# Optimization experiments

Measured on AMD Instinct MI355X. Metric: run time of the kernel, lower is better.

Reference implementation:

```python
import jax, jax.numpy as jnp
import numpy as np

B, T, C = 2, 2048, 1024
H, HS, RD = 16, 64, 64
KV_R, Q_R = 256, 384


def _rope_tables(T, dim):
    # standard RoPE angle tables, shape [T, dim]
    half = dim // 2
    inv_freq = 1.0 / (10000.0 ** (np.arange(0, half, dtype=np.float32) / half))
    t = np.arange(T, dtype=np.float32)
    ang = np.outer(t, inv_freq)  # [T, half]
    ang = np.concatenate([ang, ang], axis=-1)  # [T, dim]
    return jnp.asarray(np.cos(ang)), jnp.asarray(np.sin(ang))


def setup_inputs() -> dict:
    key = jax.random.key(0)
    ks = jax.random.split(key, 8)
    cos, sin = _rope_tables(T, RD)
    s = lambda fan_in: 1.0 / np.sqrt(fan_in)
    return {
        "x": jax.random.normal(ks[0], (B, T, C), jnp.float32),
        "cos": cos,
        "sin": sin,
        "W_kv_down": jax.random.normal(ks[1], (C, KV_R), jnp.float32) * s(C),
        "W_kv_up": jax.random.normal(ks[2], (KV_R, H * HS), jnp.float32) * s(KV_R),
        "W_k_rope": jax.random.normal(ks[3], (KV_R, H * RD), jnp.float32) * s(KV_R),
        "W_q_down": jax.random.normal(ks[4], (C, Q_R), jnp.float32) * s(C),
        "W_q_up": jax.random.normal(ks[5], (Q_R, H * HS), jnp.float32) * s(Q_R),
        "W_q_rope": jax.random.normal(ks[6], (Q_R, H * RD), jnp.float32) * s(Q_R),
        "W_out": jax.random.normal(ks[7], (H * HS, C), jnp.float32) * s(H * HS),
    }


def _apply_rope(x, cos, sin):
    # x: [B,H,T,D]; cos/sin: [T,D] broadcast
    d = x.shape[-1]
    x1, x2 = x[..., : d // 2], x[..., d // 2 :]
    rotated = jnp.concatenate([-x2, x1], axis=-1)
    return x * cos + rotated * sin


def reference(x, cos, sin, W_kv_down, W_kv_up, W_k_rope, W_q_down, W_q_up, W_q_rope, W_out):
    Bx, Tx, Cx = x.shape
    to_heads = lambda z, d: jnp.swapaxes(z.reshape(Bx, Tx, H, d), 1, 2)  # [B,H,T,d]

    latent_kv = x @ W_kv_down                      # [B,T,KV_R]
    kv_up = latent_kv @ W_kv_up                    # [B,T,H*HS]
    v = to_heads(kv_up, HS)
    k_content = to_heads(kv_up, HS)                # same projection used for k and v
    k_rope = _apply_rope(to_heads(latent_kv @ W_k_rope, RD), cos[:Tx], sin[:Tx])

    latent_q = x @ W_q_down                        # [B,T,Q_R]
    q_content = to_heads(latent_q @ W_q_up, HS)
    q_rope = _apply_rope(to_heads(latent_q @ W_q_rope, RD), cos[:Tx], sin[:Tx])

    q = jnp.concatenate([q_content, q_rope], axis=-1)  # [B,H,T,HS+RD]
    k = jnp.concatenate([k_content, k_rope], axis=-1)

    att = jnp.einsum("bhqd,bhkd->bhqk", q, k) * (HS ** -0.5)
    causal = jnp.tril(jnp.ones((Tx, Tx), bool))
    att = jnp.where(causal, att, -jnp.inf)
    att = jax.nn.softmax(att, axis=-1)             # dropout is eval-mode identity
    y = jnp.einsum("bhqk,bhkd->bhqd", att, v)      # [B,H,T,HS]
    y = jnp.swapaxes(y, 1, 2).reshape(Bx, Tx, H * HS)
    return y @ W_out
```

## Files before the change

### kernel.cpp

```cpp
#include <hip/hip_runtime.h>
#include <stdint.h>

typedef unsigned short u16;
typedef __bf16 bf16x8 __attribute__((ext_vector_type(8)));
typedef float f32x4 __attribute__((ext_vector_type(4)));

#define B_ 2
#define T_ 2048

__device__ __forceinline__ u16 f2b(float f) {
  unsigned u = __float_as_uint(f);
  u += 0x7fffu + ((u >> 16) & 1u);
  return (u16)(u >> 16);
}
__device__ __forceinline__ float b2f(u16 v) {
  return __uint_as_float(((unsigned)v) << 16);
}
__device__ __forceinline__ unsigned cvt_pk(float lo, float hi) {
  unsigned r;
  asm("v_cvt_pk_bf16_f32 %0, %1, %2" : "=v"(r) : "v"(lo), "v"(hi));
  return r;
}

using gu32 = __attribute__((address_space(1))) const unsigned int;
using lu32 = __attribute__((address_space(3))) unsigned int;
__device__ __forceinline__ void gl_lds16(const u16* g, u16* l) {
  __builtin_amdgcn_global_load_lds((gu32*)g, (lu32*)l, 16, 0, 0);
}

__global__ __launch_bounds__(256) void conv_x_kernel(const float* __restrict__ in,
                                                     u16* __restrict__ out) {
  int i = (blockIdx.x * 256 + threadIdx.x) * 4;
  float4 v = *reinterpret_cast<const float4*>(in + i);
  union { u16 h[4]; unsigned long long ll; } pk;
  pk.h[0] = f2b(v.x); pk.h[1] = f2b(v.y); pk.h[2] = f2b(v.z); pk.h[3] = f2b(v.w);
  *reinterpret_cast<unsigned long long*>(out + i) = pk.ll;
}

__global__ __launch_bounds__(256) void transpose_w_kernel(const float* __restrict__ W,
                                                          int K, int N,
                                                          u16* __restrict__ Wt,
                                                          int ldt, int row_off) {
  __shared__ float tile[32][33];
  int n0 = blockIdx.x * 32, k0 = blockIdx.y * 32;
  int cx = threadIdx.x, ry = threadIdx.y;
  #pragma unroll
  for (int i = 0; i < 4; i++)
    tile[ry + i * 8][cx] = W[(size_t)(k0 + ry + i * 8) * N + n0 + cx];
  __syncthreads();
  #pragma unroll
  for (int i = 0; i < 4; i++)
    Wt[(size_t)(row_off + n0 + ry + i * 8) * ldt + k0 + cx] = f2b(tile[cx][ry + i * 8]);
}

__global__ __launch_bounds__(256) void gemm_bt(const u16* __restrict__ A, int lda,
                                               const u16* __restrict__ Bt, int ldb,
                                               void* __restrict__ Cout, int ldc,
                                               int K, int f32out, u16* __restrict__ vt) {
  __shared__ u16 As[2][128 * 32];
  __shared__ u16 Bs[2][128 * 32];
  const int tid = threadIdx.x;
  const int wave = tid >> 6, lane = tid & 63;
  const int wr = wave >> 1, wc = wave & 1;
  const int l15 = lane & 15, l4 = lane >> 4;
  const int m0 = blockIdx.y * 128, n0 = blockIdx.x * 128;
  const int lr = lane >> 2;
  const int lc = (lane & 3) * 8;

  f32x4 acc[4][4];
  const f32x4 fzero = {0.f, 0.f, 0.f, 0.f};
  #pragma unroll
  for (int m = 0; m < 4; m++)
    #pragma unroll
    for (int n = 0; n < 4; n++)
      acc[m][n] = fzero;

  const u16* gA  = A  + (size_t)(m0 + wave * 32 + lr) * lda + lc;
  const u16* gA2 = gA + (size_t)16 * lda;
  const u16* gB  = Bt + (size_t)(n0 + wave * 32 + lr) * ldb + lc;
  const u16* gB2 = gB + (size_t)16 * ldb;

  auto stage = [&](int buf, int k0) {
    u16* lA  = &As[buf][(wave * 32) * 32];
    u16* lA2 = &As[buf][(wave * 32 + 16) * 32];
    u16* lB  = &Bs[buf][(wave * 32) * 32];
    u16* lB2 = &Bs[buf][(wave * 32 + 16) * 32];
    gl_lds16(gA + k0, lA);
    gl_lds16(gA2 + k0, lA2);
    gl_lds16(gB + k0, lB);
    gl_lds16(gB2 + k0, lB2);
  };

  stage(0, 0);
  __syncthreads();
  int buf = 0;
  for (int k0 = 0; k0 < K; k0 += 32) {
    if (k0 + 32 < K) stage(buf ^ 1, k0 + 32);
    bf16x8 af[4], bfr[4];
    #pragma unroll
    for (int m = 0; m < 4; m++)
      af[m] = *reinterpret_cast<const bf16x8*>(&As[buf][(wr * 64 + m * 16 + l15) * 32 + l4 * 8]);
    #pragma unroll
    for (int n = 0; n < 4; n++)
      bfr[n] = *reinterpret_cast<const bf16x8*>(&Bs[buf][(wc * 64 + n * 16 + l15) * 32 + l4 * 8]);
    #pragma unroll
    for (int m = 0; m < 4; m++)
      #pragma unroll
      for (int n = 0; n < 4; n++)
        acc[m][n] = __builtin_amdgcn_mfma_f32_16x16x32_bf16(af[m], bfr[n], acc[m][n], 0, 0, 0);
    __syncthreads();
    buf ^= 1;
  }

  const int row_base = m0 + wr * 64 + l4 * 4;
  const int col_base = n0 + wc * 64 + l15;
  if (f32out) {
    float* Cf = (float*)Cout;
    #pragma unroll
    for (int m = 0; m < 4; m++)
      #pragma unroll
      for (int n = 0; n < 4; n++)
        #pragma unroll
        for (int r = 0; r < 4; r++)
          Cf[(size_t)(row_base + m * 16 + r) * ldc + col_base + n * 16] = acc[m][n][r];
  } else {
    u16* Cb = (u16*)Cout;
    #pragma unroll
    for (int m = 0; m < 4; m++)
      #pragma unroll
      for (int n = 0; n < 4; n++)
        #pragma unroll
        for (int r = 0; r < 4; r++)
          Cb[(size_t)(row_base + m * 16 + r) * ldc + col_base + n * 16] = f2b(acc[m][n][r]);
    if (vt) {
      #pragma unroll
      for (int m = 0; m < 4; m++)
        #pragma unroll
        for (int n = 0; n < 4; n++) {
          int col = col_base + n * 16;
          if (col < 1024) {
            int mm = row_base + m * 16;
            int bb = mm >> 11, tt = mm & 2047;
            uint2 pk2;
            pk2.x = cvt_pk(acc[m][n][0], acc[m][n][1]);
            pk2.y = cvt_pk(acc[m][n][2], acc[m][n][3]);
            *reinterpret_cast<uint2*>(&vt[(size_t)(bb * 1024 + col) * 2048 + tt]) = pk2;
          }
        }
    }
  }
}

__global__ __launch_bounds__(256) void rope_kernel(u16* __restrict__ buf,
                                                   const float* __restrict__ cosT,
                                                   const float* __restrict__ sinT) {
  int idx = blockIdx.x * 256 + threadIdx.x;
  int i8 = (idx & 3) * 8;
  int hh = (idx >> 2) & 15;
  int r  = idx >> 6;
  int t  = r & (T_ - 1);
  size_t base = (size_t)r * 2048 + 1024 + hh * 64;
  uint4 pa = *reinterpret_cast<const uint4*>(&buf[base + i8]);
  uint4 pb = *reinterpret_cast<const uint4*>(&buf[base + i8 + 32]);
  const u16* ap = reinterpret_cast<const u16*>(&pa);
  const u16* bp = reinterpret_cast<const u16*>(&pb);
  const float* cp = cosT + t * 64 + i8;
  const float* sp = sinT + t * 64 + i8;
  float y1[8], y2[8];
  #pragma unroll
  for (int j = 0; j < 8; j++) {
    float x1 = b2f(ap[j]), x2 = b2f(bp[j]);
    y1[j] = x1 * cp[j] - x2 * sp[j];
    y2[j] = x2 * cp[j + 32] + x1 * sp[j + 32];
  }
  uint4 o1, o2;
  o1.x = cvt_pk(y1[0], y1[1]); o1.y = cvt_pk(y1[2], y1[3]);
  o1.z = cvt_pk(y1[4], y1[5]); o1.w = cvt_pk(y1[6], y1[7]);
  o2.x = cvt_pk(y2[0], y2[1]); o2.y = cvt_pk(y2[2], y2[3]);
  o2.z = cvt_pk(y2[4], y2[5]); o2.w = cvt_pk(y2[6], y2[7]);
  *reinterpret_cast<uint4*>(&buf[base + i8]) = o1;
  *reinterpret_cast<uint4*>(&buf[base + i8 + 32]) = o2;
}

__global__ __launch_bounds__(256) void attn_kernel(const u16* __restrict__ qo,
                                                   const u16* __restrict__ kvo,
                                                   const u16* __restrict__ vtg,
                                                   u16* __restrict__ yb) {
  __shared__ u16 K_lds[2][64 * 128];
  __shared__ u16 V_lds[2][64 * 64];
  __shared__ u16 P_lds[4][16][72];
  const int tid = threadIdx.x;
  const int wave = tid >> 6, lane = tid & 63;
  const int l15 = lane & 15, l4 = lane >> 4;
  const int bid = blockIdx.x;
  const int bh = bid & 31;
  const int qi = 31 - (bid >> 5);
  const int b = bh >> 4, h = bh & 15;
  const int q0 = qi * 64;
  const int qrow = q0 + wave * 16 + l15;

  const u16* qb = qo + (size_t)(b * T_ + qrow) * 2048 + h * 64;
  bf16x8 qf[4];
  qf[0] = *reinterpret_cast<const bf16x8*>(qb + l4 * 8);
  qf[1] = *reinterpret_cast<const bf16x8*>(qb + 32 + l4 * 8);
  qf[2] = *reinterpret_cast<const bf16x8*>(qb + 1024 + l4 * 8);
  qf[3] = *reinterpret_cast<const bf16x8*>(qb + 1056 + l4 * 8);

  const u16* Kbase = kvo + (size_t)(b * T_) * 2048 + h * 64;
  const u16* Vbase = vtg + (size_t)(b * 1024 + h * 64) * 2048;

  const int krow_i = lane >> 4;
  const int kc2 = (lane & 15) * 16;
  const int vrow_i = lane >> 3;
  const int vc2 = (lane & 7) * 16;

  auto stage = [&](int buf, int kv0) {
    #pragma unroll
    for (int j = 0; j < 4; j++) {
      int row = wave * 16 + j * 4 + krow_i;
      int c2x = kc2 ^ ((row & 7) << 4);
      int cu = c2x >> 1;
      const u16* src = Kbase + (size_t)(kv0 + row) * 2048 + (cu < 64 ? cu : 960 + cu);
      gl_lds16(src, &K_lds[buf][(wave * 16 + j * 4) * 128]);
    }
    #pragma unroll
    for (int j = 0; j < 2; j++) {
      int row = wave * 16 + j * 8 + vrow_i;
      int c2x = vc2 ^ ((row & 7) << 4);
      const u16* src = Vbase + (size_t)row * 2048 + kv0 + (c2x >> 1);
      gl_lds16(src, &V_lds[buf][(wave * 16 + j * 8) * 64]);
    }
  };

  const f32x4 fzero = {0.f, 0.f, 0.f, 0.f};
  f32x4 oT[4];
  #pragma unroll
  for (int f = 0; f < 4; f++) oT[f] = fzero;
  float m_run = -1e30f, l_run = 0.f;

  const int nt = qi + 1;
  stage(0, 0);
  __syncthreads();
  int buf = 0;

  for (int t = 0; t < nt; t++) {
    const int kv0 = t * 64;
    if (t + 1 < nt) stage(buf ^ 1, kv0 + 64);

    const char* Kb = (const char*)&K_lds[buf][0];
    const char* Vb = (const char*)&V_lds[buf][0];

    f32x4 sT[4];
    #pragma unroll
    for (int c = 0; c < 4; c++) sT[c] = fzero;
    #pragma unroll
    for (int c = 0; c < 4; c++) {
      const int krow = c * 16 + l15;
      const int kxm = (krow & 7) << 4;
      #pragma unroll
      for (int s = 0; s < 4; s++) {
        bf16x8 kf = *reinterpret_cast<const bf16x8*>(
            Kb + krow * 256 + ((s * 64 + l4 * 16) ^ kxm));
        sT[c] = __builtin_amdgcn_mfma_f32_16x16x32_bf16(kf, qf[s], sT[c], 0, 0, 0);
      }
    }

    const bool diag = (kv0 == q0);
    float p[4][4];
    float mx = -1e30f;
    #pragma unroll
    for (int c = 0; c < 4; c++)
      #pragma unroll
      for (int r = 0; r < 4; r++) {
        float s = sT[c][r] * 0.125f;
        if (diag) {
          int kv = kv0 + c * 16 + l4 * 4 + r;
          if (kv > qrow) s = -1e30f;
        }
        p[c][r] = s;
        mx = fmaxf(mx, s);
      }
    mx = fmaxf(mx, __shfl_xor(mx, 16));
    mx = fmaxf(mx, __shfl_xor(mx, 32));
    float m_new = fmaxf(m_run, mx);
    float corr = __expf(m_run - m_new);
    float rsum = 0.f;
    #pragma unroll
    for (int c = 0; c < 4; c++)
      #pragma unroll
      for (int r = 0; r < 4; r++) {
        float pe = __expf(p[c][r] - m_new);
        p[c][r] = pe;
        rsum += pe;
      }
    rsum += __shfl_xor(rsum, 16);
    rsum += __shfl_xor(rsum, 32);
    l_run = l_run * corr + rsum;
    m_run = m_new;
    #pragma unroll
    for (int f = 0; f < 4; f++) oT[f] *= corr;

    #pragma unroll
    for (int c = 0; c < 4; c++) {
      uint2 pk2;
      pk2.x = cvt_pk(p[c][0], p[c][1]);
      pk2.y = cvt_pk(p[c][2], p[c][3]);
      *reinterpret_cast<uint2*>(&P_lds[wave][l15][c * 16 + l4 * 4]) = pk2;
    }
    bf16x8 pb0 = *reinterpret_cast<const bf16x8*>(&P_lds[wave][l15][l4 * 8]);
    bf16x8 pb1 = *reinterpret_cast<const bf16x8*>(&P_lds[wave][l15][32 + l4 * 8]);

    #pragma unroll
    for (int f = 0; f < 4; f++) {
      const int vrow = f * 16 + l15;
      const int vxm = (vrow & 7) << 4;
      bf16x8 v0 = *reinterpret_cast<const bf16x8*>(Vb + vrow * 128 + ((l4 * 16) ^ vxm));
      bf16x8 v1 = *reinterpret_cast<const bf16x8*>(Vb + vrow * 128 + ((64 + l4 * 16) ^ vxm));
      oT[f] = __builtin_amdgcn_mfma_f32_16x16x32_bf16(v0, pb0, oT[f], 0, 0, 0);
      oT[f] = __builtin_amdgcn_mfma_f32_16x16x32_bf16(v1, pb1, oT[f], 0, 0, 0);
    }

    __syncthreads();
    buf ^= 1;
  }

  const float inv = 1.f / l_run;
  #pragma unroll
  for (int f = 0; f < 4; f++) {
    uint2 pk2;
    pk2.x = cvt_pk(oT[f][0] * inv, oT[f][1] * inv);
    pk2.y = cvt_pk(oT[f][2] * inv, oT[f][3] * inv);
    *reinterpret_cast<uint2*>(
        &yb[(size_t)(b * T_ + qrow) * 1024 + h * 64 + f * 16 + l4 * 4]) = pk2;
  }
}

extern "C" void kernel_launch(void* const* d_in, const int* in_sizes, int n_in,
                              void* d_out, int out_size, void* d_ws, size_t ws_size,
                              hipStream_t stream) {
  const float* x         = (const float*)d_in[0];
  const float* cosT      = (const float*)d_in[1];
  const float* sinT      = (const float*)d_in[2];
  const float* W_kv_down = (const float*)d_in[3];
  const float* W_kv_up   = (const float*)d_in[4];
  const float* W_k_rope  = (const float*)d_in[5];
  const float* W_q_down  = (const float*)d_in[6];
  const float* W_q_up    = (const float*)d_in[7];
  const float* W_q_rope  = (const float*)d_in[8];
  const float* W_out     = (const float*)d_in[9];
  float* out = (float*)d_out;
  char* ws = (char*)d_ws;

  u16* xb    = (u16*)(ws + 0);
  u16* lat   = (u16*)(ws + 8388608);
  u16* WdT   = (u16*)(ws + 13631488);
  u16* WkvT  = (u16*)(ws + 14942208);
  u16* WqT   = (u16*)(ws + 15990784);
  u16* WoutT = (u16*)(ws + 17563648);
  u16* kvo   = (u16*)(ws + 19660800);
  u16* qo    = (u16*)(ws + 36438016);
  u16* VT    = (u16*)(ws + 53215232);
  u16* yb    = (u16*)(ws + 0);

  dim3 tb(32, 8);
  conv_x_kernel<<<4096, 256, 0, stream>>>(x, xb);
  transpose_w_kernel<<<dim3(8, 32),  tb, 0, stream>>>(W_kv_down, 1024, 256,  WdT,  1024, 0);
  transpose_w_kernel<<<dim3(12, 32), tb, 0, stream>>>(W_q_down,  1024, 384,  WdT,  1024, 256);
  transpose_w_kernel<<<dim3(32, 8),  tb, 0, stream>>>(W_kv_up,   256,  1024, WkvT, 256,  0);
  transpose_w_kernel<<<dim3(32, 8),  tb, 0, stream>>>(W_k_rope,  256,  1024, WkvT, 256,  1024);
  transpose_w_kernel<<<dim3(32, 12), tb, 0, stream>>>(W_q_up,    384,  1024, WqT,  384,  0);
  transpose_w_kernel<<<dim3(32, 12), tb, 0, stream>>>(W_q_rope,  384,  1024, WqT,  384,  1024);
  transpose_w_kernel<<<dim3(32, 32), tb, 0, stream>>>(W_out,     1024, 1024, WoutT, 1024, 0);

  gemm_bt<<<dim3(5, 32), 256, 0, stream>>>(xb, 1024, WdT, 1024, lat, 640, 1024, 0, nullptr);
  gemm_bt<<<dim3(16, 32), 256, 0, stream>>>(lat, 640, WkvT, 256, kvo, 2048, 256, 0, VT);
  gemm_bt<<<dim3(16, 32), 256, 0, stream>>>(lat + 256, 640, WqT, 384, qo, 2048, 384, 0, nullptr);

  rope_kernel<<<1024, 256, 0, stream>>>(kvo, cosT, sinT);
  rope_kernel<<<1024, 256, 0, stream>>>(qo, cosT, sinT);

  attn_kernel<<<1024, 256, 0, stream>>>(qo, kvo, VT, yb);

  gemm_bt<<<dim3(8, 32), 256, 0, stream>>>(yb, 1024, WoutT, 1024, out, 1024, 1024, 1, nullptr);
}
```

Before: 248.9 us.

## Fuse RoPE into GEMM epilogue, batch transposes, enlarge attention tiles, lazy rescale

The seven weight transposes are merged into one launch driven by a job table. RoPE moves into the epilogue of the up-projection GEMMs, which removes the separate read-modify-write rope pass. Attention now uses 512-thread blocks covering 128 query rows and shares each K/V tile across eight waves, skipping tiles above the diagonal per wave. Softmax switches to exp2 with a pre-scaled logit and only rescales when the running max rises past a threshold. The gain comes from fewer launches and less global traffic, at the cost of wave imbalance near the diagonal and a looser softmax rescale that could affect precision.

```diff
diff --git a/kernel.cpp b/kernel.cpp
--- a/kernel.cpp
+++ b/kernel.cpp
@@ -19,6 +19,11 @@
 __device__ __forceinline__ unsigned cvt_pk(float lo, float hi) {
   unsigned r;
   asm("v_cvt_pk_bf16_f32 %0, %1, %2" : "=v"(r) : "v"(lo), "v"(hi));
+  return r;
+}
+__device__ __forceinline__ float ex2(float x) {
+  float r;
+  asm("v_exp_f32 %0, %1" : "=v"(r) : "v"(x));
   return r;
 }
 
@@ -37,26 +42,37 @@
   *reinterpret_cast<unsigned long long*>(out + i) = pk.ll;
 }
 
-__global__ __launch_bounds__(256) void transpose_w_kernel(const float* __restrict__ W,
-                                                          int K, int N,
-                                                          u16* __restrict__ Wt,
-                                                          int ldt, int row_off) {
+struct TJob { const float* src; u16* dst; int K, N, ldt, row_off, blk0; };
+struct TJobs { TJob j[7]; };
+
+__global__ __launch_bounds__(256) void transpose_all_kernel(TJobs jobs) {
   __shared__ float tile[32][33];
-  int n0 = blockIdx.x * 32, k0 = blockIdx.y * 32;
+  int bid = blockIdx.x;
+  int ji = 0;
+  #pragma unroll
+  for (int i = 6; i > 0; --i)
+    if (bid >= jobs.j[i].blk0) { ji = i; break; }
+  const TJob jb = jobs.j[ji];
+  int local = bid - jb.blk0;
+  int nb = jb.N >> 5;
+  int n0 = (local % nb) * 32, k0 = (local / nb) * 32;
   int cx = threadIdx.x, ry = threadIdx.y;
   #pragma unroll
   for (int i = 0; i < 4; i++)
-    tile[ry + i * 8][cx] = W[(size_t)(k0 + ry + i * 8) * N + n0 + cx];
+    tile[ry + i * 8][cx] = jb.src[(size_t)(k0 + ry + i * 8) * jb.N + n0 + cx];
   __syncthreads();
   #pragma unroll
   for (int i = 0; i < 4; i++)
-    Wt[(size_t)(row_off + n0 + ry + i * 8) * ldt + k0 + cx] = f2b(tile[cx][ry + i * 8]);
+    jb.dst[(size_t)(jb.row_off + n0 + ry + i * 8) * jb.ldt + k0 + cx] =
+        f2b(tile[cx][ry + i * 8]);
 }
 
 __global__ __launch_bounds__(256) void gemm_bt(const u16* __restrict__ A, int lda,
                                                const u16* __restrict__ Bt, int ldb,
                                                void* __restrict__ Cout, int ldc,
-                                               int K, int f32out, u16* __restrict__ vt) {
+                                               int K, int mode, u16* __restrict__ vt,
+                                               const float* __restrict__ cosT,
+                                               const float* __restrict__ sinT) {
   __shared__ u16 As[2][128 * 32];
   __shared__ u16 Bs[2][128 * 32];
   const int tid = threadIdx.x;
@@ -81,14 +97,10 @@
   const u16* gB2 = gB + (size_t)16 * ldb;
 
   auto stage = [&](int buf, int k0) {
-    u16* lA  = &As[buf][(wave * 32) * 32];
-    u16* lA2 = &As[buf][(wave * 32 + 16) * 32];
-    u16* lB  = &Bs[buf][(wave * 32) * 32];
-    u16* lB2 = &Bs[buf][(wave * 32 + 16) * 32];
-    gl_lds16(gA + k0, lA);
-    gl_lds16(gA2 + k0, lA2);
-    gl_lds16(gB + k0, lB);
-    gl_lds16(gB2 + k0, lB2);
+    gl_lds16(gA + k0, &As[buf][(wave * 32) * 32]);
+    gl_lds16(gA2 + k0, &As[buf][(wave * 32 + 16) * 32]);
+    gl_lds16(gB + k0, &Bs[buf][(wave * 32) * 32]);
+    gl_lds16(gB2 + k0, &Bs[buf][(wave * 32 + 16) * 32]);
   };
 
   stage(0, 0);
@@ -114,7 +126,8 @@
 
   const int row_base = m0 + wr * 64 + l4 * 4;
   const int col_base = n0 + wc * 64 + l15;
-  if (f32out) {
+
+  if (mode == 1) {
     float* Cf = (float*)Cout;
     #pragma unroll
     for (int m = 0; m < 4; m++)
@@ -123,80 +136,70 @@
         #pragma unroll
         for (int r = 0; r < 4; r++)
           Cf[(size_t)(row_base + m * 16 + r) * ldc + col_base + n * 16] = acc[m][n][r];
-  } else {
-    u16* Cb = (u16*)Cout;
-    #pragma unroll
-    for (int m = 0; m < 4; m++)
-      #pragma unroll
-      for (int n = 0; n < 4; n++)
-        #pragma unroll
-        for (int r = 0; r < 4; r++)
-          Cb[(size_t)(row_base + m * 16 + r) * ldc + col_base + n * 16] = f2b(acc[m][n][r]);
-    if (vt) {
-      #pragma unroll
-      for (int m = 0; m < 4; m++)
-        #pragma unroll
-        for (int n = 0; n < 4; n++) {
-          int col = col_base + n * 16;
-          if (col < 1024) {
-            int mm = row_base + m * 16;
-            int bb = mm >> 11, tt = mm & 2047;
-            uint2 pk2;
-            pk2.x = cvt_pk(acc[m][n][0], acc[m][n][1]);
-            pk2.y = cvt_pk(acc[m][n][2], acc[m][n][3]);
-            *reinterpret_cast<uint2*>(&vt[(size_t)(bb * 1024 + col) * 2048 + tt]) = pk2;
-          }
+    return;
+  }
+
+  if (mode >= 2 && (n0 + wc * 64) >= 1024) {
+    #pragma unroll
+    for (int m = 0; m < 4; m++)
+      #pragma unroll
+      for (int r = 0; r < 4; r++) {
+        int t = (row_base + m * 16 + r) & (T_ - 1);
+        const float* cp = cosT + t * 64 + l15;
+        const float* sp = sinT + t * 64 + l15;
+        float c0 = cp[0], c16 = cp[16], c32 = cp[32], c48 = cp[48];
+        float s0 = sp[0], s16 = sp[16], s32 = sp[32], s48 = sp[48];
+        float x0 = acc[m][0][r], x1 = acc[m][1][r];
+        float x2 = acc[m][2][r], x3 = acc[m][3][r];
+        acc[m][0][r] = x0 * c0 - x2 * s0;
+        acc[m][1][r] = x1 * c16 - x3 * s16;
+        acc[m][2][r] = x2 * c32 + x0 * s32;
+        acc[m][3][r] = x3 * c48 + x1 * s48;
+      }
+  }
+
+  u16* Cb = (u16*)Cout;
+  #pragma unroll
+  for (int m = 0; m < 4; m++)
+    #pragma unroll
+    for (int n = 0; n < 4; n++)
+      #pragma unroll
+      for (int r = 0; r < 4; r++)
+        Cb[(size_t)(row_base + m * 16 + r) * ldc + col_base + n * 16] = f2b(acc[m][n][r]);
+
+  if (mode == 2) {
+    #pragma unroll
+    for (int m = 0; m < 4; m++)
+      #pragma unroll
+      for (int n = 0; n < 4; n++) {
+        int col = col_base + n * 16;
+        if (col < 1024) {
+          int mm = row_base + m * 16;
+          int bb = mm >> 11, tt = mm & 2047;
+          uint2 pk2;
+          pk2.x = cvt_pk(acc[m][n][0], acc[m][n][1]);
+          pk2.y = cvt_pk(acc[m][n][2], acc[m][n][3]);
+          *reinterpret_cast<uint2*>(&vt[(size_t)(bb * 1024 + col) * 2048 + tt]) = pk2;
         }
-    }
-  }
-}
-
-__global__ __launch_bounds__(256) void rope_kernel(u16* __restrict__ buf,
-                                                   const float* __restrict__ cosT,
-                                                   const float* __restrict__ sinT) {
-  int idx = blockIdx.x * 256 + threadIdx.x;
-  int i8 = (idx & 3) * 8;
-  int hh = (idx >> 2) & 15;
-  int r  = idx >> 6;
-  int t  = r & (T_ - 1);
-  size_t base = (size_t)r * 2048 + 1024 + hh * 64;
-  uint4 pa = *reinterpret_cast<const uint4*>(&buf[base + i8]);
-  uint4 pb = *reinterpret_cast<const uint4*>(&buf[base + i8 + 32]);
-  const u16* ap = reinterpret_cast<const u16*>(&pa);
-  const u16* bp = reinterpret_cast<const u16*>(&pb);
-  const float* cp = cosT + t * 64 + i8;
-  const float* sp = sinT + t * 64 + i8;
-  float y1[8], y2[8];
-  #pragma unroll
-  for (int j = 0; j < 8; j++) {
-    float x1 = b2f(ap[j]), x2 = b2f(bp[j]);
-    y1[j] = x1 * cp[j] - x2 * sp[j];
-    y2[j] = x2 * cp[j + 32] + x1 * sp[j + 32];
-  }
-  uint4 o1, o2;
-  o1.x = cvt_pk(y1[0], y1[1]); o1.y = cvt_pk(y1[2], y1[3]);
-  o1.z = cvt_pk(y1[4], y1[5]); o1.w = cvt_pk(y1[6], y1[7]);
-  o2.x = cvt_pk(y2[0], y2[1]); o2.y = cvt_pk(y2[2], y2[3]);
-  o2.z = cvt_pk(y2[4], y2[5]); o2.w = cvt_pk(y2[6], y2[7]);
-  *reinterpret_cast<uint4*>(&buf[base + i8]) = o1;
-  *reinterpret_cast<uint4*>(&buf[base + i8 + 32]) = o2;
-}
-
-__global__ __launch_bounds__(256) void attn_kernel(const u16* __restrict__ qo,
+      }
+  }
+}
+
+__global__ __launch_bounds__(512) void attn_kernel(const u16* __restrict__ qo,
                                                    const u16* __restrict__ kvo,
                                                    const u16* __restrict__ vtg,
                                                    u16* __restrict__ yb) {
   __shared__ u16 K_lds[2][64 * 128];
   __shared__ u16 V_lds[2][64 * 64];
-  __shared__ u16 P_lds[4][16][72];
+  __shared__ u16 P_lds[8][16][72];
   const int tid = threadIdx.x;
   const int wave = tid >> 6, lane = tid & 63;
   const int l15 = lane & 15, l4 = lane >> 4;
   const int bid = blockIdx.x;
   const int bh = bid & 31;
-  const int qi = 31 - (bid >> 5);
+  const int qi = 15 - (bid >> 5);
   const int b = bh >> 4, h = bh & 15;
-  const int q0 = qi * 64;
+  const int q0 = qi * 128;
   const int qrow = q0 + wave * 16 + l15;
 
   const u16* qb = qo + (size_t)(b * T_ + qrow) * 2048 + h * 64;
@@ -216,19 +219,18 @@
 
   auto stage = [&](int buf, int kv0) {
     #pragma unroll
-    for (int j = 0; j < 4; j++) {
-      int row = wave * 16 + j * 4 + krow_i;
+    for (int j = 0; j < 2; j++) {
+      int row = wave * 8 + j * 4 + krow_i;
       int c2x = kc2 ^ ((row & 7) << 4);
       int cu = c2x >> 1;
       const u16* src = Kbase + (size_t)(kv0 + row) * 2048 + (cu < 64 ? cu : 960 + cu);
-      gl_lds16(src, &K_lds[buf][(wave * 16 + j * 4) * 128]);
+      gl_lds16(src, &K_lds[buf][(wave * 8 + j * 4) * 128]);
     }
-    #pragma unroll
-    for (int j = 0; j < 2; j++) {
-      int row = wave * 16 + j * 8 + vrow_i;
+    {
+      int row = wave * 8 + vrow_i;
       int c2x = vc2 ^ ((row & 7) << 4);
       const u16* src = Vbase + (size_t)row * 2048 + kv0 + (c2x >> 1);
-      gl_lds16(src, &V_lds[buf][(wave * 16 + j * 8) * 64]);
+      gl_lds16(src, &V_lds[buf][(wave * 8) * 64]);
     }
   };
 
@@ -238,7 +240,10 @@
   for (int f = 0; f < 4; f++) oT[f] = fzero;
   float m_run = -1e30f, l_run = 0.f;
 
-  const int nt = qi + 1;
+  const float SCALE2 = 0.125f * 1.44269504f;
+  const int nt = qi * 2 + 2;
+  const int t_diag = qi * 2 + (wave >> 2);
+
   stage(0, 0);
   __syncthreads();
   int buf = 0;
@@ -247,77 +252,82 @@
     const int kv0 = t * 64;
     if (t + 1 < nt) stage(buf ^ 1, kv0 + 64);
 
-    const char* Kb = (const char*)&K_lds[buf][0];
-    const char* Vb = (const char*)&V_lds[buf][0];
-
-    f32x4 sT[4];
-    #pragma unroll
-    for (int c = 0; c < 4; c++) sT[c] = fzero;
-    #pragma unroll
-    for (int c = 0; c < 4; c++) {
-      const int krow = c * 16 + l15;
-      const int kxm = (krow & 7) << 4;
-      #pragma unroll
-      for (int s = 0; s < 4; s++) {
-        bf16x8 kf = *reinterpret_cast<const bf16x8*>(
-            Kb + krow * 256 + ((s * 64 + l4 * 16) ^ kxm));
-        sT[c] = __builtin_amdgcn_mfma_f32_16x16x32_bf16(kf, qf[s], sT[c], 0, 0, 0);
-      }
-    }
-
-    const bool diag = (kv0 == q0);
-    float p[4][4];
-    float mx = -1e30f;
-    #pragma unroll
-    for (int c = 0; c < 4; c++)
-      #pragma unroll
-      for (int r = 0; r < 4; r++) {
-        float s = sT[c][r] * 0.125f;
-        if (diag) {
-          int kv = kv0 + c * 16 + l4 * 4 + r;
-          if (kv > qrow) s = -1e30f;
+    if (t <= t_diag) {
+      const char* Kb = (const char*)&K_lds[buf][0];
+      const char* Vb = (const char*)&V_lds[buf][0];
+
+      f32x4 sT[4];
+      #pragma unroll
+      for (int c = 0; c < 4; c++) sT[c] = fzero;
+      #pragma unroll
+      for (int c = 0; c < 4; c++) {
+        const int krow = c * 16 + l15;
+        const int kxm = (krow & 7) << 4;
+        #pragma unroll
+        for (int s = 0; s < 4; s++) {
+          bf16x8 kf = *reinterpret_cast<const bf16x8*>(
+              Kb + krow * 256 + ((s * 64 + l4 * 16) ^ kxm));
+          sT[c] = __builtin_amdgcn_mfma_f32_16x16x32_bf16(kf, qf[s], sT[c], 0, 0, 0);
         }
-        p[c][r] = s;
-        mx = fmaxf(mx, s);
-      }
-    mx = fmaxf(mx, __shfl_xor(mx, 16));
-    mx = fmaxf(mx, __shfl_xor(mx, 32));
-    float m_new = fmaxf(m_run, mx);
-    float corr = __expf(m_run - m_new);
-    float rsum = 0.f;
-    #pragma unroll
-    for (int c = 0; c < 4; c++)
-      #pragma unroll
-      for (int r = 0; r < 4; r++) {
-        float pe = __expf(p[c][r] - m_new);
-        p[c][r] = pe;
-        rsum += pe;
-      }
-    rsum += __shfl_xor(rsum, 16);
-    rsum += __shfl_xor(rsum, 32);
-    l_run = l_run * corr + rsum;
-    m_run = m_new;
-    #pragma unroll
-    for (int f = 0; f < 4; f++) oT[f] *= corr;
-
-    #pragma unroll
-    for (int c = 0; c < 4; c++) {
-      uint2 pk2;
-      pk2.x = cvt_pk(p[c][0], p[c][1]);
-      pk2.y = cvt_pk(p[c][2], p[c][3]);
-      *reinterpret_cast<uint2*>(&P_lds[wave][l15][c * 16 + l4 * 4]) = pk2;
-    }
-    bf16x8 pb0 = *reinterpret_cast<const bf16x8*>(&P_lds[wave][l15][l4 * 8]);
-    bf16x8 pb1 = *reinterpret_cast<const bf16x8*>(&P_lds[wave][l15][32 + l4 * 8]);
-
-    #pragma unroll
-    for (int f = 0; f < 4; f++) {
-      const int vrow = f * 16 + l15;
-      const int vxm = (vrow & 7) << 4;
-      bf16x8 v0 = *reinterpret_cast<const bf16x8*>(Vb + vrow * 128 + ((l4 * 16) ^ vxm));
-      bf16x8 v1 = *reinterpret_cast<const bf16x8*>(Vb + vrow * 128 + ((64 + l4 * 16) ^ vxm));
-      oT[f] = __builtin_amdgcn_mfma_f32_16x16x32_bf16(v0, pb0, oT[f], 0, 0, 0);
-      oT[f] = __builtin_amdgcn_mfma_f32_16x16x32_bf16(v1, pb1, oT[f], 0, 0, 0);
+      }
+
+      const bool diag = (t == t_diag);
+      float p[4][4];
+      float mx = -1e30f;
+      #pragma unroll
+      for (int c = 0; c < 4; c++)
+        #pragma unroll
+        for (int r = 0; r < 4; r++) {
+          float s = sT[c][r] * SCALE2;
+          if (diag) {
+            int kv = kv0 + c * 16 + l4 * 4 + r;
+            if (kv > qrow) s = -1e30f;
+          }
+          p[c][r] = s;
+          mx = fmaxf(mx, s);
+        }
+      mx = fmaxf(mx, __shfl_xor(mx, 16));
+      mx = fmaxf(mx, __shfl_xor(mx, 32));
+      if (__any(mx > m_run + 11.5f)) {
+        float m_new = fmaxf(m_run, mx);
+        float corr = ex2(m_run - m_new);
+        l_run *= corr;
+        #pragma unroll
+        for (int f = 0; f < 4; f++) oT[f] *= corr;
+        m_run = m_new;
+      }
+      float rsum = 0.f;
+      #pragma unroll
+      for (int c = 0; c < 4; c++)
+        #pragma unroll
+        for (int r = 0; r < 4; r++) {
+          float pe = ex2(p[c][r] - m_run);
+          p[c][r] = pe;
+          rsum += pe;
+        }
+      rsum += __shfl_xor(rsum, 16);
+      rsum += __shfl_xor(rsum, 32);
+      l_run += rsum;
+
+      #pragma unroll
+      for (int c = 0; c < 4; c++) {
+        uint2 pk2;
+        pk2.x = cvt_pk(p[c][0], p[c][1]);
+        pk2.y = cvt_pk(p[c][2], p[c][3]);
+        *reinterpret_cast<uint2*>(&P_lds[wave][l15][c * 16 + l4 * 4]) = pk2;
+      }
+      bf16x8 pb0 = *reinterpret_cast<const bf16x8*>(&P_lds[wave][l15][l4 * 8]);
+      bf16x8 pb1 = *reinterpret_cast<const bf16x8*>(&P_lds[wave][l15][32 + l4 * 8]);
+
+      #pragma unroll
+      for (int f = 0; f < 4; f++) {
+        const int vrow = f * 16 + l15;
+        const int vxm = (vrow & 7) << 4;
+        bf16x8 v0 = *reinterpret_cast<const bf16x8*>(Vb + vrow * 128 + ((l4 * 16) ^ vxm));
+        bf16x8 v1 = *reinterpret_cast<const bf16x8*>(Vb + vrow * 128 + ((64 + l4 * 16) ^ vxm));
+        oT[f] = __builtin_amdgcn_mfma_f32_16x16x32_bf16(v0, pb0, oT[f], 0, 0, 0);
+        oT[f] = __builtin_amdgcn_mfma_f32_16x16x32_bf16(v1, pb1, oT[f], 0, 0, 0);
+      }
     }
 
     __syncthreads();
@@ -362,24 +372,27 @@
   u16* VT    = (u16*)(ws + 53215232);
   u16* yb    = (u16*)(ws + 0);
 
-  dim3 tb(32, 8);
   conv_x_kernel<<<4096, 256, 0, stream>>>(x, xb);
-  transpose_w_kernel<<<dim3(8, 32),  tb, 0, stream>>>(W_kv_down, 1024, 256,  WdT,  1024, 0);
-  transpose_w_kernel<<<dim3(12, 32), tb, 0, stream>>>(W_q_down,  1024, 384,  WdT,  1024, 256);
-  transpose_w_kernel<<<dim3(32, 8),  tb, 0, stream>>>(W_kv_up,   256,  1024, WkvT, 256,  0);
-  transpose_w_kernel<<<dim3(32, 8),  tb, 0, stream>>>(W_k_rope,  256,  1024, WkvT, 256,  1024);
-  transpose_w_kernel<<<dim3(32, 12), tb, 0, stream>>>(W_q_up,    384,  1024, WqT,  384,  0);
-  transpose_w_kernel<<<dim3(32, 12), tb, 0, stream>>>(W_q_rope,  384,  1024, WqT,  384,  1024);
-  transpose_w_kernel<<<dim3(32, 32), tb, 0, stream>>>(W_out,     1024, 1024, WoutT, 1024, 0);
-
-  gemm_bt<<<dim3(5, 32), 256, 0, stream>>>(xb, 1024, WdT, 1024, lat, 640, 1024, 0, nullptr);
-  gemm_bt<<<dim3(16, 32), 256, 0, stream>>>(lat, 640, WkvT, 256, kvo, 2048, 256, 0, VT);
-  gemm_bt<<<dim3(16, 32), 256, 0, stream>>>(lat + 256, 640, WqT, 384, qo, 2048, 384, 0, nullptr);
-
-  rope_kernel<<<1024, 256, 0, stream>>>(kvo, cosT, sinT);
-  rope_kernel<<<1024, 256, 0, stream>>>(qo, cosT, sinT);
-
-  attn_kernel<<<1024, 256, 0, stream>>>(qo, kvo, VT, yb);
-
-  gemm_bt<<<dim3(8, 32), 256, 0, stream>>>(yb, 1024, WoutT, 1024, out, 1024, 1024, 1, nullptr);
-}
+
+  TJobs jobs;
+  jobs.j[0] = {W_kv_down, WdT,   1024, 256,  1024, 0,    0};
+  jobs.j[1] = {W_q_down,  WdT,   1024, 384,  1024, 256,  256};
+  jobs.j[2] = {W_kv_up,   WkvT,  256,  1024, 256,  0,    640};
+  jobs.j[3] = {W_k_rope,  WkvT,  256,  1024, 256,  1024, 896};
+  jobs.j[4] = {W_q_up,    WqT,   384,  1024, 384,  0,    1152};
+  jobs.j[5] = {W_q_rope,  WqT,   384,  1024, 384,  1024, 1536};
+  jobs.j[6] = {W_out,     WoutT, 1024, 1024, 1024, 0,    1920};
+  transpose_all_kernel<<<2944, dim3(32, 8), 0, stream>>>(jobs);
+
+  gemm_bt<<<dim3(5, 32), 256, 0, stream>>>(xb, 1024, WdT, 1024, lat, 640, 1024, 0,
+                                           nullptr, nullptr, nullptr);
+  gemm_bt<<<dim3(16, 32), 256, 0, stream>>>(lat, 640, WkvT, 256, kvo, 2048, 256, 2,
+                                            VT, cosT, sinT);
+  gemm_bt<<<dim3(16, 32), 256, 0, stream>>>(lat + 256, 640, WqT, 384, qo, 2048, 384, 3,
+                                            nullptr, cosT, sinT);
+
+  attn_kernel<<<512, 512, 0, stream>>>(qo, kvo, VT, yb);
+
+  gemm_bt<<<dim3(8, 32), 256, 0, stream>>>(yb, 1024, WoutT, 1024, out, 1024, 1024, 1,
+                                           nullptr, nullptr, nullptr);
+}
```

New measurement: 231.0 us. -7.2%, faster.
